# Kernel optimization log

Hardware: AMD Instinct MI355X
Metric: run time of the kernel (lower is better)

## Reference

```python
import jax, jax.numpy as jnp
import numpy as np

SEQ, D, H = 4096, 1024, 16
HD = D // H
SCALE = HD ** -0.5


def setup_inputs() -> dict:
    key = jax.random.key(0)
    ks = jax.random.split(key, 8)
    s = 0.02
    return {
        "hidden_states": jax.random.normal(ks[0], (SEQ, D), dtype=jnp.float32),
        "wq": jax.random.normal(ks[1], (D, D), dtype=jnp.float32) * s,
        "bq": jax.random.normal(ks[2], (D,), dtype=jnp.float32) * s,
        "wk": jax.random.normal(ks[3], (D, D), dtype=jnp.float32) * s,
        "wv": jax.random.normal(ks[4], (D, D), dtype=jnp.float32) * s,
        "bv": jax.random.normal(ks[5], (D,), dtype=jnp.float32) * s,
        "wo": jax.random.normal(ks[6], (D, D), dtype=jnp.float32) * s,
        "bo": jax.random.normal(ks[7], (D,), dtype=jnp.float32) * s,
    }


def reference(hidden_states, wq, bq, wk, wv, bv, wo, bo):
    S = hidden_states.shape[0]
    # torch Linear: y = x @ W^T + b  (k_proj has no bias)
    q = (hidden_states @ wq.T + bq).reshape(S, H, HD).transpose(1, 0, 2)  # [H,S,hd]
    k = (hidden_states @ wk.T).reshape(S, H, HD).transpose(1, 0, 2)       # [H,S,hd]
    v = (hidden_states @ wv.T + bv).reshape(S, H, HD).transpose(1, 0, 2)  # [H,S,hd]
    scores = jnp.einsum('hqd,hkd->hqk', q, k) * SCALE                     # [H,S,S]
    # softmax computed in fp32 then cast back to query dtype
    attn = jax.nn.softmax(scores.astype(jnp.float32), axis=-1).astype(q.dtype)
    out = jnp.einsum('hqk,hkd->hqd', attn, v)                             # [H,S,hd]
    out = out.transpose(1, 0, 2).reshape(S, D)
    return out @ wo.T + bo
```

## Files before the change

kernel.cpp:

```cpp
#include <hip/hip_runtime.h>

#define SEQ 4096
#define DIM 1024
#define NH 16
#define HD 64
#define QKVSTR 3072

typedef __attribute__((ext_vector_type(8))) short bf16x8;
typedef __attribute__((ext_vector_type(4))) float f32x4;
typedef __attribute__((ext_vector_type(16))) float f32x16;
typedef __attribute__((ext_vector_type(4))) unsigned int uint4v;

__device__ __forceinline__ unsigned short f2bf(float f) {
  unsigned int b = __float_as_uint(f);
  b = b + 0x7fffu + ((b >> 16) & 1u);
  return (unsigned short)(b >> 16);
}

__device__ __forceinline__ unsigned int cvt_pk_bf16(float lo, float hi) {
  unsigned int r;
  asm("v_cvt_pk_bf16_f32 %0, %1, %2" : "=v"(r) : "v"(lo), "v"(hi));
  return r;
}

__device__ __forceinline__ float fast_exp2(float x) {
#if __has_builtin(__builtin_amdgcn_exp2f)
  return __builtin_amdgcn_exp2f(x);
#else
  float r; asm("v_exp_f32 %0, %1" : "=v"(r) : "v"(x)); return r;
#endif
}

typedef __attribute__((address_space(3))) unsigned int lds_uint;
typedef __attribute__((address_space(1))) const unsigned int global_uint;

__device__ __forceinline__ void gload_lds16(const void* g, void* l) {
  __builtin_amdgcn_global_load_lds((global_uint*)g, (lds_uint*)l, 16, 0, 0);
}

__global__ __launch_bounds__(256) void cast_all_kernel(
    const float* __restrict__ X, const float* __restrict__ wq, const float* __restrict__ wk,
    const float* __restrict__ wv, const float* __restrict__ wo,
    unsigned short* __restrict__ Xb, unsigned short* __restrict__ Wqkv,
    unsigned short* __restrict__ Wob, float qscale) {
  int i = blockIdx.x * 256 + threadIdx.x;
  const float* src;
  unsigned short* dst;
  float sc = 1.f;
  if (i < 524288) { src = X + (size_t)i * 8; dst = Xb + (size_t)i * 8; }
  else if (i < 655360) { int j = i - 524288; src = wq + (size_t)j * 8; dst = Wqkv + (size_t)j * 8; sc = qscale; }
  else if (i < 786432) { int j = i - 655360; src = wk + (size_t)j * 8; dst = Wqkv + 1048576 + (size_t)j * 8; }
  else if (i < 917504) { int j = i - 786432; src = wv + (size_t)j * 8; dst = Wqkv + 2097152 + (size_t)j * 8; }
  else { int j = i - 917504; src = wo + (size_t)j * 8; dst = Wob + (size_t)j * 8; }
  const float4* p = (const float4*)src;
  float4 x0 = p[0], x1 = p[1];
  union { unsigned short u[8]; uint4v v; } o;
  o.u[0] = f2bf(x0.x * sc); o.u[1] = f2bf(x0.y * sc);
  o.u[2] = f2bf(x0.z * sc); o.u[3] = f2bf(x0.w * sc);
  o.u[4] = f2bf(x1.x * sc); o.u[5] = f2bf(x1.y * sc);
  o.u[6] = f2bf(x1.z * sc); o.u[7] = f2bf(x1.w * sc);
  *(uint4v*)dst = o.v;
}

template<int BIASMODE, int OUT_F32, int BN>
__global__ __launch_bounds__(256) void gemm_bt_kernel(
    const unsigned short* __restrict__ A, const unsigned short* __restrict__ B,
    const float* __restrict__ b0, const float* __restrict__ b1, float qscale,
    void* __restrict__ Cout, unsigned short* __restrict__ Vt, int M, int N, int K) {
  constexpr int NF = BN / 32;
  __shared__ unsigned short As[2][128 * 32];
  __shared__ unsigned short Bs[2][BN * 32];
  int tid = threadIdx.x;
  int wave = tid >> 6, lane = tid & 63;
  int g = lane >> 4, lc = lane & 15;
  int wm = wave >> 1, wn = wave & 1;

  int gx = gridDim.x;
  int wgid = blockIdx.y * gx + blockIdx.x;
  int cpx = (gx * gridDim.y) >> 3;
  int sw = (wgid & 7) * cpx + (wgid >> 3);
  int m0 = (sw / gx) * 128, n0 = (sw % gx) * BN;

  int ch0 = wave * 64 + lane;
  int r0 = ch0 >> 2, cb0 = ch0 & 3;
  int ch1 = 256 + ch0;
  int r1 = ch1 >> 2, cb1 = ch1 & 3;
  const unsigned short* Ar0 = A + (size_t)(m0 + r0) * K + cb0 * 8;
  const unsigned short* Ar1 = A + (size_t)(m0 + r1) * K + cb1 * 8;
  const unsigned short* Br0 = B + (size_t)(n0 + r0) * K + cb0 * 8;
  const unsigned short* Br1 = B + (size_t)(n0 + r1) * K + cb1 * 8;
  unsigned short* sAlo[2] = { &As[0][(wave * 64) * 8],       &As[1][(wave * 64) * 8] };
  unsigned short* sAhi[2] = { &As[0][(256 + wave * 64) * 8], &As[1][(256 + wave * 64) * 8] };
  unsigned short* sBlo[2] = { &Bs[0][(wave * 64) * 8],       &Bs[1][(wave * 64) * 8] };
  unsigned short* sBhi[2] = { &Bs[0][(256 + wave * 64) * 8], &Bs[1][(256 + wave * 64) * 8] };

  f32x4 acc[4][NF] = {};

  gload_lds16(Ar0, sAlo[0]);
  gload_lds16(Ar1, sAhi[0]);
  gload_lds16(Br0, sBlo[0]);
  if (BN == 128) gload_lds16(Br1, sBhi[0]);

  int cur = 0;
  for (int k0 = 0; k0 < K; k0 += 32) {
    {
      int kn = (k0 + 32 < K) ? (k0 + 32) : 0;
      int nb = cur ^ 1;
      gload_lds16(Ar0 + kn, sAlo[nb]);
      gload_lds16(Ar1 + kn, sAhi[nb]);
      gload_lds16(Br0 + kn, sBlo[nb]);
      if (BN == 128) gload_lds16(Br1 + kn, sBhi[nb]);
    }
    if (BN == 128) {
      asm volatile("s_waitcnt vmcnt(4)" ::: "memory");
    } else {
      asm volatile("s_waitcnt vmcnt(3)" ::: "memory");
    }
    __builtin_amdgcn_sched_barrier(0);
    __builtin_amdgcn_s_barrier();
    __builtin_amdgcn_sched_barrier(0);

    bf16x8 af[4], bfr[NF];
    for (int mf = 0; mf < 4; ++mf)
      af[mf] = *(const bf16x8*)&As[cur][(wm * 64 + mf * 16 + lc) * 32 + g * 8];
    for (int nf = 0; nf < NF; ++nf)
      bfr[nf] = *(const bf16x8*)&Bs[cur][(wn * (BN / 2) + nf * 16 + lc) * 32 + g * 8];
    for (int mf = 0; mf < 4; ++mf)
      for (int nf = 0; nf < NF; ++nf)
        acc[mf][nf] = __builtin_amdgcn_mfma_f32_16x16x32_bf16(af[mf], bfr[nf], acc[mf][nf], 0, 0, 0);

    asm volatile("" ::: "memory");
    __builtin_amdgcn_sched_barrier(0);
    __builtin_amdgcn_s_barrier();
    cur ^= 1;
  }

  for (int nf = 0; nf < NF; ++nf) {
    int col = n0 + wn * (BN / 2) + nf * 16 + lc;
    float bias = 0.f;
    if (BIASMODE == 1) {
      int sect = col >> 10, cc = col & 1023;
      bias = (sect == 0) ? b0[cc] * qscale : ((sect == 2) ? b1[cc] : 0.f);
    } else if (BIASMODE == 2) {
      bias = b0[col];
    }
    for (int mf = 0; mf < 4; ++mf) {
      int row = m0 + wm * 64 + mf * 16 + g * 4;
      for (int r = 0; r < 4; ++r) {
        float v = acc[mf][nf][r] + bias;
        if (OUT_F32) {
          ((float*)Cout)[(size_t)(row + r) * N + col] = v;
        } else if (BIASMODE == 1 && col >= 2048) {
          Vt[(size_t)(col - 2048) * SEQ + row + r] = f2bf(v);
        } else {
          ((unsigned short*)Cout)[(size_t)(row + r) * N + col] = f2bf(v);
        }
      }
    }
  }
}

__global__ __launch_bounds__(512, 1) void attn_kernel(
    const unsigned short* __restrict__ QKV, const unsigned short* __restrict__ Vt,
    unsigned short* __restrict__ Aout) {
  __shared__ unsigned short Qs[128 * 64];
  __shared__ unsigned short Ks[2][2][64 * 64];
  __shared__ unsigned short Vs[2][2][64 * 64];
  int tid = threadIdx.x;
  int w = tid >> 6, lane = tid & 63;
  int hi = lane >> 5, l31 = lane & 31;
  int qw = w & 3, grp = w >> 2;

  int bid = blockIdx.x;
  int swz = (bid & 7) * 64 + (bid >> 3);
  int h = swz >> 5;
  int q0 = (swz & 31) * 128;

  const unsigned short* Qg = QKV + h * HD;
  const unsigned short* Kg = QKV + DIM + h * HD;
  const unsigned short* Vg = Vt + (size_t)(h * HD) * SEQ;
  int kvbase = grp * (SEQ / 2);

  int ch0 = qw * 64 + lane;
  int r0s = ch0 >> 3, d0s = (ch0 & 7) ^ (r0s & 7);
  int ch1 = 256 + ch0;
  int r1s = ch1 >> 3, d1s = (ch1 & 7) ^ (r1s & 7);
  size_t koff0 = (size_t)r0s * QKVSTR + d0s * 8;
  size_t koff1 = (size_t)r1s * QKVSTR + d1s * 8;
  size_t voff0 = (size_t)r0s * SEQ + d0s * 8;
  size_t voff1 = (size_t)r1s * SEQ + d1s * 8;
  unsigned short* sKlo[2] = { &Ks[grp][0][(qw * 64) * 8],       &Ks[grp][1][(qw * 64) * 8] };
  unsigned short* sKhi[2] = { &Ks[grp][0][(256 + qw * 64) * 8], &Ks[grp][1][(256 + qw * 64) * 8] };
  unsigned short* sVlo[2] = { &Vs[grp][0][(qw * 64) * 8],       &Vs[grp][1][(qw * 64) * 8] };
  unsigned short* sVhi[2] = { &Vs[grp][0][(256 + qw * 64) * 8], &Vs[grp][1][(256 + qw * 64) * 8] };

  for (int c = 0; c < 2; ++c) {
    int chunk = c * 512 + w * 64 + lane;
    int row = chunk >> 3, pos = chunk & 7;
    int db = pos ^ (row & 7);
    gload_lds16(Qg + (size_t)(q0 + row) * QKVSTR + db * 8, Qs + (c * 512 + w * 64) * 8);
  }
  {
    const unsigned short* Kt = Kg + (size_t)kvbase * QKVSTR;
    const unsigned short* Vtt = Vg + kvbase;
    gload_lds16(Kt + koff0, sKlo[0]);
    gload_lds16(Kt + koff1, sKhi[0]);
    gload_lds16(Vtt + voff0, sVlo[0]);
    gload_lds16(Vtt + voff1, sVhi[0]);
  }
  asm volatile("s_waitcnt vmcnt(4)" ::: "memory");
  __builtin_amdgcn_sched_barrier(0);
  __builtin_amdgcn_s_barrier();

  bf16x8 qf[4];
  {
    int qrow = qw * 32 + l31;
    for (int dc = 0; dc < 4; ++dc) {
      int pos = 2 * dc + hi;
      qf[dc] = *(const bf16x8*)&Qs[qrow * 64 + (pos ^ (qrow & 7)) * 8];
    }
  }

  int offb[4];
#pragma unroll
  for (int dc = 0; dc < 4; ++dc)
    offb[dc] = l31 * 128 + (((2 * dc + hi) ^ (l31 & 7)) * 16);
  const char* KbA = (const char*)&Ks[grp][0][0];
  const char* KbB = (const char*)&Ks[grp][1][0];
  const char* VbA = (const char*)&Vs[grp][0][0];
  const char* VbB = (const char*)&Vs[grp][1][0];

  f32x16 o0 = {}, o1 = {};
  float la0 = 0.f, la1 = 0.f, la2 = 0.f, la3 = 0.f;

  auto body = [&](int t, int CUR) {
    int NB = CUR ^ 1;
    int kvn = kvbase + (((t + 1) & 31) << 6);
    const unsigned short* Kt = Kg + (size_t)kvn * QKVSTR;
    const unsigned short* Vtt = Vg + kvn;
    gload_lds16(Kt + koff0, sKlo[NB]);
    gload_lds16(Kt + koff1, sKhi[NB]);
    gload_lds16(Vtt + voff0, sVlo[NB]);
    gload_lds16(Vtt + voff1, sVhi[NB]);
    asm volatile("s_waitcnt vmcnt(4)" ::: "memory");
    __builtin_amdgcn_sched_barrier(0);
    __builtin_amdgcn_s_barrier();
    __builtin_amdgcn_sched_barrier(0);

    const char* Kb = CUR ? KbB : KbA;
    const char* Vb = CUR ? VbB : VbA;
    bf16x8 kf0[4], kf1[4];
#pragma unroll
    for (int dc = 0; dc < 4; ++dc) {
      kf0[dc] = *(const bf16x8*)(Kb + offb[dc]);
      kf1[dc] = *(const bf16x8*)(Kb + offb[dc] + 4096);
    }
    f32x16 st0 = {}, st1 = {};
    __builtin_amdgcn_s_setprio(1);
#pragma unroll
    for (int dc = 0; dc < 4; ++dc) {
      st0 = __builtin_amdgcn_mfma_f32_32x32x16_bf16(kf0[dc], qf[dc], st0, 0, 0, 0);
      st1 = __builtin_amdgcn_mfma_f32_32x32x16_bf16(kf1[dc], qf[dc], st1, 0, 0, 0);
    }
    __builtin_amdgcn_s_setprio(0);

    bf16x8 vf0[4], vf1[4];
#pragma unroll
    for (int c = 0; c < 4; ++c) {
      vf0[c] = *(const bf16x8*)(Vb + offb[c]);
      vf1[c] = *(const bf16x8*)(Vb + offb[c] + 4096);
    }

    float p0[16], p1[16];
#pragma unroll
    for (int r = 0; r < 16; r += 4) {
      p0[r] = fast_exp2(st0[r]); p0[r + 1] = fast_exp2(st0[r + 1]);
      p0[r + 2] = fast_exp2(st0[r + 2]); p0[r + 3] = fast_exp2(st0[r + 3]);
      la0 += p0[r]; la1 += p0[r + 1]; la2 += p0[r + 2]; la3 += p0[r + 3];
    }
#pragma unroll
    for (int r = 0; r < 16; r += 4) {
      p1[r] = fast_exp2(st1[r]); p1[r + 1] = fast_exp2(st1[r + 1]);
      p1[r + 2] = fast_exp2(st1[r + 2]); p1[r + 3] = fast_exp2(st1[r + 3]);
      la0 += p1[r]; la1 += p1[r + 1]; la2 += p1[r + 2]; la3 += p1[r + 3];
    }

    bf16x8 pa[4];
#pragma unroll
    for (int f = 0; f < 2; ++f) {
      const float* pp = f ? p1 : p0;
#pragma unroll
      for (int cc = 0; cc < 2; ++cc) {
        unsigned uLO0 = cvt_pk_bf16(pp[8 * cc + 0], pp[8 * cc + 1]);
        unsigned uLO1 = cvt_pk_bf16(pp[8 * cc + 2], pp[8 * cc + 3]);
        unsigned uHI0 = cvt_pk_bf16(pp[8 * cc + 4], pp[8 * cc + 5]);
        unsigned uHI1 = cvt_pk_bf16(pp[8 * cc + 6], pp[8 * cc + 7]);
        auto s0 = __builtin_amdgcn_permlane32_swap(uLO0, uHI0, false, false);
        auto s1 = __builtin_amdgcn_permlane32_swap(uLO1, uHI1, false, false);
        union { unsigned u[4]; bf16x8 v; } pw;
        pw.u[0] = s0[0]; pw.u[1] = s1[0]; pw.u[2] = s0[1]; pw.u[3] = s1[1];
        pa[f * 2 + cc] = pw.v;
      }
    }

    __builtin_amdgcn_s_setprio(1);
#pragma unroll
    for (int c = 0; c < 4; ++c) {
      o0 = __builtin_amdgcn_mfma_f32_32x32x16_bf16(pa[c], vf0[c], o0, 0, 0, 0);
      o1 = __builtin_amdgcn_mfma_f32_32x32x16_bf16(pa[c], vf1[c], o1, 0, 0, 0);
    }
    __builtin_amdgcn_s_setprio(0);

    asm volatile("" ::: "memory");
    __builtin_amdgcn_sched_barrier(0);
    __builtin_amdgcn_s_barrier();
  };

  for (int tt = 0; tt < 32; tt += 2) {
    body(tt + 0, 0);
    body(tt + 1, 1);
  }

  float lsum = (la0 + la1) + (la2 + la3);
  lsum += __shfl_xor(lsum, 32);

  __syncthreads();
  float* cbO0 = (float*)&Ks[0][0][0];
  float* cbO1 = (float*)&Vs[0][0][0];
  float* cbL  = (float*)&Qs[0];
  int cbase = (qw * 64 + lane) * 32;
  int lx = lane & 31;
  if (grp == 1) {
#pragma unroll
    for (int r = 0; r < 16; ++r) {
      cbO0[cbase + (r ^ lx)] = o0[r];
      cbO1[cbase + (r ^ lx)] = o1[r];
    }
    cbL[qw * 64 + lane] = lsum;
  }
  __syncthreads();
  if (grp == 0) {
#pragma unroll
    for (int r = 0; r < 16; ++r) {
      o0[r] += cbO0[cbase + (r ^ lx)];
      o1[r] += cbO1[cbase + (r ^ lx)];
    }
    lsum += cbL[qw * 64 + lane];
    float inv = 1.f / lsum;
#pragma unroll
    for (int r = 0; r < 16; ++r) {
      int qr = (r & 3) + 8 * (r >> 2) + 4 * hi;
      float ir = __shfl(inv, qr + (lane & 32));
      size_t row = q0 + qw * 32 + qr;
      Aout[row * DIM + h * HD + l31]      = f2bf(o0[r] * ir);
      Aout[row * DIM + h * HD + 32 + l31] = f2bf(o1[r] * ir);
    }
  }
}

extern "C" void kernel_launch(void* const* d_in, const int* in_sizes, int n_in,
                              void* d_out, int out_size, void* d_ws, size_t ws_size,
                              hipStream_t stream) {
  (void)in_sizes; (void)n_in; (void)out_size; (void)ws_size;
  const float* X  = (const float*)d_in[0];
  const float* wq = (const float*)d_in[1];
  const float* bq = (const float*)d_in[2];
  const float* wk = (const float*)d_in[3];
  const float* wv = (const float*)d_in[4];
  const float* bv = (const float*)d_in[5];
  const float* wo = (const float*)d_in[6];
  const float* bo = (const float*)d_in[7];

  char* ws = (char*)d_ws;
  const size_t SZ_XD  = (size_t)SEQ * DIM * 2;
  const size_t SZ_W   = (size_t)DIM * DIM * 2;
  const size_t SZ_QKV = (size_t)SEQ * QKVSTR * 2;
  unsigned short* Xb   = (unsigned short*)(ws);
  unsigned short* Wqkv = (unsigned short*)(ws + SZ_XD);
  unsigned short* Wob  = (unsigned short*)(ws + SZ_XD + 3 * SZ_W);
  unsigned short* QKVb = (unsigned short*)(ws + SZ_XD + 4 * SZ_W);
  unsigned short* Vtb  = (unsigned short*)(ws + SZ_XD + 4 * SZ_W + SZ_QKV);
  unsigned short* Ab   = Xb;

  const float QSCALE = 0.125f * 1.44269504088896f;

  cast_all_kernel<<<4096, 256, 0, stream>>>(X, wq, wk, wv, wo, Xb, Wqkv, Wob, QSCALE);

  gemm_bt_kernel<1, 0, 128><<<dim3(QKVSTR / 128, SEQ / 128), 256, 0, stream>>>(
      Xb, Wqkv, bq, bv, QSCALE, QKVb, Vtb, SEQ, QKVSTR, DIM);

  attn_kernel<<<SEQ / 128 * NH, 512, 0, stream>>>(QKVb, Vtb, Ab);

  gemm_bt_kernel<2, 1, 64><<<dim3(DIM / 64, SEQ / 128), 256, 0, stream>>>(
      Ab, Wob, bo, nullptr, 1.f, d_out, nullptr, SEQ, DIM, DIM);
}
```

Measured before the change: 162.0 us.

## Triple-buffer GEMM LDS tiles to prefetch two K-steps ahead

Turns the GEMM main loop's double-buffered global-to-LDS pipeline into a triple-buffered one. Loads are issued two K-tiles ahead and the loop is unrolled by three so buffer indices are compile-time constants. The aim is to hide more global memory latency behind the MFMA work. In exchange it uses 1.5x the LDS, which may reduce occupancy, and the loop now hardcodes 32 K-steps, so K must equal 1024.

Result: no change. 159.7 us (-1.4%).

```diff
diff --git a/kernel.cpp b/kernel.cpp
--- a/kernel.cpp
+++ b/kernel.cpp
@@ -68,8 +68,8 @@
     const float* __restrict__ b0, const float* __restrict__ b1, float qscale,
     void* __restrict__ Cout, unsigned short* __restrict__ Vt, int M, int N, int K) {
   constexpr int NF = BN / 32;
-  __shared__ unsigned short As[2][128 * 32];
-  __shared__ unsigned short Bs[2][BN * 32];
+  __shared__ unsigned short As[3][128 * 32];
+  __shared__ unsigned short Bs[3][BN * 32];
   int tid = threadIdx.x;
   int wave = tid >> 6, lane = tid & 63;
   int g = lane >> 4, lc = lane & 15;
@@ -89,51 +89,60 @@
   const unsigned short* Ar1 = A + (size_t)(m0 + r1) * K + cb1 * 8;
   const unsigned short* Br0 = B + (size_t)(n0 + r0) * K + cb0 * 8;
   const unsigned short* Br1 = B + (size_t)(n0 + r1) * K + cb1 * 8;
-  unsigned short* sAlo[2] = { &As[0][(wave * 64) * 8],       &As[1][(wave * 64) * 8] };
-  unsigned short* sAhi[2] = { &As[0][(256 + wave * 64) * 8], &As[1][(256 + wave * 64) * 8] };
-  unsigned short* sBlo[2] = { &Bs[0][(wave * 64) * 8],       &Bs[1][(wave * 64) * 8] };
-  unsigned short* sBhi[2] = { &Bs[0][(256 + wave * 64) * 8], &Bs[1][(256 + wave * 64) * 8] };
+
+  unsigned short* sAlo[3] = { &As[0][(wave * 64) * 8], &As[1][(wave * 64) * 8], &As[2][(wave * 64) * 8] };
+  unsigned short* sAhi[3] = { &As[0][(256 + wave * 64) * 8], &As[1][(256 + wave * 64) * 8], &As[2][(256 + wave * 64) * 8] };
+  unsigned short* sBlo[3] = { &Bs[0][(wave * 64) * 8], &Bs[1][(wave * 64) * 8], &Bs[2][(wave * 64) * 8] };
+  unsigned short* sBhi[3] = { &Bs[0][(256 + wave * 64) * 8], &Bs[1][(256 + wave * 64) * 8], &Bs[2][(256 + wave * 64) * 8] };
 
   f32x4 acc[4][NF] = {};
 
-  gload_lds16(Ar0, sAlo[0]);
-  gload_lds16(Ar1, sAhi[0]);
-  gload_lds16(Br0, sBlo[0]);
-  if (BN == 128) gload_lds16(Br1, sBhi[0]);
-
-  int cur = 0;
-  for (int k0 = 0; k0 < K; k0 += 32) {
-    {
-      int kn = (k0 + 32 < K) ? (k0 + 32) : 0;
-      int nb = cur ^ 1;
-      gload_lds16(Ar0 + kn, sAlo[nb]);
-      gload_lds16(Ar1 + kn, sAhi[nb]);
-      gload_lds16(Br0 + kn, sBlo[nb]);
-      if (BN == 128) gload_lds16(Br1 + kn, sBhi[nb]);
-    }
-    if (BN == 128) {
-      asm volatile("s_waitcnt vmcnt(4)" ::: "memory");
-    } else {
-      asm volatile("s_waitcnt vmcnt(3)" ::: "memory");
-    }
-    __builtin_amdgcn_sched_barrier(0);
-    __builtin_amdgcn_s_barrier();
-    __builtin_amdgcn_sched_barrier(0);
-
+  auto stage = [&](int kn, int b) {
+    gload_lds16(Ar0 + kn, sAlo[b]);
+    gload_lds16(Ar1 + kn, sAhi[b]);
+    gload_lds16(Br0 + kn, sBlo[b]);
+    if (BN == 128) gload_lds16(Br1 + kn, sBhi[b]);
+  };
+
+  auto compute = [&](int b) {
     bf16x8 af[4], bfr[NF];
     for (int mf = 0; mf < 4; ++mf)
-      af[mf] = *(const bf16x8*)&As[cur][(wm * 64 + mf * 16 + lc) * 32 + g * 8];
+      af[mf] = *(const bf16x8*)&As[b][(wm * 64 + mf * 16 + lc) * 32 + g * 8];
     for (int nf = 0; nf < NF; ++nf)
-      bfr[nf] = *(const bf16x8*)&Bs[cur][(wn * (BN / 2) + nf * 16 + lc) * 32 + g * 8];
+      bfr[nf] = *(const bf16x8*)&Bs[b][(wn * (BN / 2) + nf * 16 + lc) * 32 + g * 8];
     for (int mf = 0; mf < 4; ++mf)
       for (int nf = 0; nf < NF; ++nf)
         acc[mf][nf] = __builtin_amdgcn_mfma_f32_16x16x32_bf16(af[mf], bfr[nf], acc[mf][nf], 0, 0, 0);
-
+  };
+
+  const int NT = K / 32;
+  auto step = [&](int i, int CUR, int STG) {
+    int kn = (i + 2 < NT) ? (i + 2) * 32 : 0;
+    stage(kn, STG);
+    if (BN == 128) {
+      asm volatile("s_waitcnt vmcnt(8)" ::: "memory");
+    } else {
+      asm volatile("s_waitcnt vmcnt(6)" ::: "memory");
+    }
+    __builtin_amdgcn_sched_barrier(0);
+    __builtin_amdgcn_s_barrier();
+    __builtin_amdgcn_sched_barrier(0);
+    compute(CUR);
     asm volatile("" ::: "memory");
     __builtin_amdgcn_sched_barrier(0);
     __builtin_amdgcn_s_barrier();
-    cur ^= 1;
-  }
+  };
+
+  stage(0, 0);
+  stage(32, 1);
+
+  for (int ii = 0; ii < 30; ii += 3) {
+    step(ii + 0, 0, 2);
+    step(ii + 1, 1, 0);
+    step(ii + 2, 2, 1);
+  }
+  step(30, 0, 2);
+  step(31, 1, 0);
 
   for (int nf = 0; nf < NF; ++nf) {
     int col = n0 + wn * (BN / 2) + nf * 16 + lc;
```
